# Performance work log

Hardware: AMD Instinct MI355X
Metric: run time of the kernel (lower is better)

## Reference

```python
import jax, jax.numpy as jnp
import numpy as np

OUT = 7  # STN crop size hard-coded as (7, 7) in the original build()


def gather_pairs(num_points):
    # replicates the pred_gather_indexes construction in build()
    pairs = [[0, 0]]
    si = 1
    while si + 2 < num_points:
        pairs.append([si, si])
        pairs.append([si + 1, si + 2])
        si += 3
    pairs.append([si, si])
    pairs.append([si + 1, si + 1])
    return np.asarray(pairs, dtype=np.int32)


def _sample_one(feat, theta):
    # feat [H,W,C], theta [6] = affine row-major 2x3; classic STN bilinear crop
    H, W, _ = feat.shape
    lin = jnp.linspace(-1.0, 1.0, OUT)
    gy, gx = jnp.meshgrid(lin, lin, indexing='ij')
    xs = theta[0] * gx + theta[1] * gy + theta[2]
    ys = theta[3] * gx + theta[4] * gy + theta[5]
    px = (xs + 1.0) * (W - 1) * 0.5
    py = (ys + 1.0) * (H - 1) * 0.5
    x0 = jnp.floor(px)
    y0 = jnp.floor(py)
    wx = px - x0
    wy = py - y0
    x0i = jnp.clip(x0, 0, W - 1).astype(jnp.int32)
    x1i = jnp.clip(x0 + 1, 0, W - 1).astype(jnp.int32)
    y0i = jnp.clip(y0, 0, H - 1).astype(jnp.int32)
    y1i = jnp.clip(y0 + 1, 0, H - 1).astype(jnp.int32)
    Ia = feat[y0i, x0i]
    Ib = feat[y1i, x0i]
    Ic = feat[y0i, x1i]
    Id = feat[y1i, x1i]
    wa = ((1 - wx) * (1 - wy))[..., None]
    wb = ((1 - wx) * wy)[..., None]
    wc = (wx * (1 - wy))[..., None]
    wd = (wx * wy)[..., None]
    return wa * Ia + wb * Ib + wc * Ic + wd * Id  # [OUT,OUT,C]

# vmap over boxes then over batch -> feat [B,H,W,C], theta [B,n,6] -> [B,n,7,7,C]
_sample = jax.vmap(jax.vmap(_sample_one, in_axes=(None, 0)), in_axes=(0, 0))


def _hierarchy(pred_prev, feat, W1, b1, W2, b2, W3, b3):
    B = pred_prev.shape[0]
    centers = (pred_prev[:, :-1] + pred_prev[:, 1:]) * 0.5
    diffs = (pred_prev[:, 1:] - pred_prev[:, :-1]) * 0.5
    cx, cy = centers[..., 0], centers[..., 1]
    dx, dy = diffs[..., 0], diffs[..., 1]
    # fixed (non-trainable) dense with constant kernel -> theta = [dx,-dy,-cx,dy,dx,-cy]
    theta = jnp.stack([dx, -dy, -cx, dy, dx, -cy], axis=-1)  # [B,n,6]
    theta = jax.lax.stop_gradient(theta)  # stop_gradient=True default
    rois = _sample(feat, theta)  # [B,n,7,7,C]
    n = theta.shape[1]
    x = rois.reshape(B * n, -1)
    f1 = jnp.tanh(x @ W1 + b1)
    f2 = jnp.tanh(f1 @ W2 + b2)
    f3 = f2 @ W3 + b3 + jnp.asarray([-1.0, 0.0, 0.0, 0.0, 1.0, 0.0], dtype=f2.dtype)
    npnt = n * 3
    pts = f3.reshape(B, npnt, 2)
    # fixed homography dense: (x,y) -> (x,y,-1)
    hom = jnp.concatenate([pts, -jnp.ones((B, npnt, 1), dtype=pts.dtype)], axis=-1)
    theta_e = jnp.repeat(theta, 3, axis=1).reshape(B, npnt, 2, 3)
    pt = jnp.einsum('bpij,bpj->bpi', theta_e, hom)  # [B,npnt,2]
    idx = gather_pairs(npnt)  # [m,2]
    pg = pt[:, idx]  # [B,m,2,2]
    return pg.mean(axis=2)  # [B,m,2]


def setup_inputs() -> dict:
    key = jax.random.key(0)
    ks = jax.random.split(key, 16)
    B = 32
    d = {
        'last_feature': jax.random.normal(ks[0], (B, 4096), jnp.float32),
        'conv4_3': jax.random.normal(ks[1], (B, 28, 28, 512), jnp.float32),
        'conv3_3': jax.random.normal(ks[2], (B, 56, 56, 256), jnp.float32),
        'conv2_2': jax.random.normal(ks[3], (B, 112, 112, 128), jnp.float32),
        'W_trans': jax.random.normal(ks[4], (4096, 18), jnp.float32) * 0.005,
        'b_trans': jnp.zeros((18,), jnp.float32),
    }
    C = [512, 256, 128]
    for h in range(3):
        kk = jax.random.split(ks[5 + h], 3)
        fan = OUT * OUT * C[h]
        d[f'W1_{h}'] = jax.random.normal(kk[0], (fan, 1024), jnp.float32) * 0.001
        d[f'b1_{h}'] = jnp.zeros((1024,), jnp.float32)
        d[f'W2_{h}'] = jax.random.normal(kk[1], (1024, 256), jnp.float32) * 0.02
        d[f'b2_{h}'] = jnp.zeros((256,), jnp.float32)
        d[f'W3_{h}'] = jax.random.normal(kk[2], (256, 6), jnp.float32) * 0.01
        d[f'b3_{h}'] = jnp.zeros((6,), jnp.float32)
    return d


def reference(last_feature, conv4_3, conv3_3, conv2_2, W_trans, b_trans,
              W1_0, b1_0, W2_0, b2_0, W3_0, b3_0,
              W1_1, b1_1, W2_1, b2_1, W3_1, b3_1,
              W1_2, b1_2, W2_2, b2_2, W3_2, b3_2):
    B = last_feature.shape[0]
    pred = (last_feature @ W_trans + b_trans).reshape(B, 9, 2)
    feats = [conv4_3, conv3_3, conv2_2]
    heads = [(W1_0, b1_0, W2_0, b2_0, W3_0, b3_0),
             (W1_1, b1_1, W2_1, b2_1, W3_1, b3_1),
             (W1_2, b1_2, W2_2, b2_2, W3_2, b3_2)]
    for h in range(3):
        pred = _hierarchy(pred, feats[h], *heads[h])
    return pred[:, :-1, :] * 6.0  # [B,64,2]
```

## Files before the change

kernel.cpp:

```cpp
#include <hip/hip_runtime.h>
#include <hip/hip_bf16.h>
#include <math.h>

typedef __attribute__((ext_vector_type(8))) short   short8;
typedef __attribute__((ext_vector_type(4))) float   floatx4;

#define OFF_PRED     0ULL
#define OFF_PTA      16384ULL
#define OFF_PTB      65536ULL
#define OFF_W2T      131072ULL
#define OFF_F1       2097152ULL
#define OFF_P2       4194304ULL
#define OFF_X        16777216ULL
#define OFF_P1       33554432ULL
#define OFF_W1T      67108864ULL

__device__ inline void pair_idx(int p, int Pn, int npnt, int& i1, int& i2) {
    if (p == 0) { i1 = i2 = 0; }
    else if (p >= Pn - 2) { i1 = i2 = npnt - (Pn - p); }
    else {
        int q = (p - 1) >> 1, r = (p - 1) & 1;
        int si = 1 + 3 * q;
        if (r == 0) { i1 = i2 = si; } else { i1 = si + 1; i2 = si + 2; }
    }
}
__device__ inline float2 pred_point(const float* pred0, const float* pt,
                                    int nsegP, int b, int p) {
    if (nsegP == 0) {
        const float* q = pred0 + ((size_t)b * 9 + p) * 2;
        return float2{q[0], q[1]};
    }
    int npnt = nsegP * 3, Pn = 2 * nsegP + 1;
    int i1, i2; pair_idx(p, Pn, npnt, i1, i2);
    const float* a = pt + ((size_t)b * npnt + i1) * 2;
    const float* c = pt + ((size_t)b * npnt + i2) * 2;
    return float2{0.5f * (a[0] + c[0]), 0.5f * (a[1] + c[1])};
}

struct SetupArgs {
    const float* W1s[3]; __hip_bfloat16* W1T[3]; int K[3];
    const float* W2s[3]; __hip_bfloat16* W2T[3];
    const float* lf; const float* Wt; const float* bt; float* pred;
};

__device__ inline void transpose_tile(const float* __restrict__ src,
                                      __hip_bfloat16* __restrict__ dst,
                                      int R, int C, int rowT, int colT,
                                      float (*tile)[33]) {
    int tx = threadIdx.x & 31, ty = threadIdx.x >> 5;
    int r0 = rowT * 32, c0 = colT * 32;
    #pragma unroll
    for (int k = 0; k < 4; ++k)
        tile[ty + k * 8][tx] = src[(size_t)(r0 + ty + k * 8) * C + c0 + tx];
    __syncthreads();
    #pragma unroll
    for (int k = 0; k < 4; ++k)
        dst[(size_t)(c0 + ty + k * 8) * R + r0 + tx] =
            __float2bfloat16(tile[tx][ty + k * 8]);
}

__global__ __launch_bounds__(256) void setup_kernel(SetupArgs a) {
    __shared__ float tile[32][33];
    int id = blockIdx.x;
    if (id < 43904) {
        int h = (id < 25088) ? 0 : (id < 37632 ? 1 : 2);
        int base = (h == 0) ? 0 : (h == 1 ? 25088 : 37632);
        int l = id - base;
        transpose_tile(a.W1s[h], a.W1T[h], a.K[h], 1024, l >> 5, l & 31, tile);
    } else if (id < 44672) {
        int l = id - 43904;
        int h = l >> 8; int t = l & 255;
        transpose_tile(a.W2s[h], a.W2T[h], 1024, 256, t >> 3, t & 7, tile);
    } else {
        int l = id - 44672;
        int wave = threadIdx.x >> 6, lane = threadIdx.x & 63;
        int task = l * 4 + wave;
        int j = task % 18, b = task / 18;
        const float* lfb = a.lf + (size_t)b * 4096;
        float acc = 0.f;
        for (int k = lane; k < 4096; k += 64)
            acc += lfb[k] * a.Wt[(size_t)k * 18 + j];
        #pragma unroll
        for (int off = 32; off >= 1; off >>= 1)
            acc += __shfl_xor(acc, off, 64);
        if (lane == 0) a.pred[b * 18 + j] = acc + a.bt[j];
    }
}

__global__ __launch_bounds__(256) void sample_kernel(
    const float* __restrict__ feat, int Wd, int lc,
    const float* __restrict__ pred0, const float* __restrict__ ptPrev, int nsegP,
    int lns, __hip_bfloat16* __restrict__ x)
{
    int nseg = 1 << lns;
    int blk = blockIdx.x;
    int i = blk & (nseg - 1), b = blk >> lns;
    float2 p0 = pred_point(pred0, ptPrev, nsegP, b, i);
    float2 p1 = pred_point(pred0, ptPrev, nsegP, b, i + 1);
    float cx = 0.5f * (p0.x + p1.x), cy = 0.5f * (p0.y + p1.y);
    float dx = 0.5f * (p1.x - p0.x), dy = 0.5f * (p1.y - p0.y);

    __shared__ float4 wv[49];
    __shared__ int4   ov[49];
    int t = threadIdx.x;
    int C = 1 << lc;
    if (t < 49) {
        int oy = t / 7, ox = t - oy * 7;
        float gx = (float)(ox - 3) * (1.f / 3.f);
        float gy = (float)(oy - 3) * (1.f / 3.f);
        float xs = dx * gx - dy * gy - cx;
        float ys = dy * gx + dx * gy - cy;
        float fW = (float)(Wd - 1);
        float px = (xs + 1.f) * fW * 0.5f;
        float py = (ys + 1.f) * fW * 0.5f;
        float x0f = floorf(px), y0f = floorf(py);
        float wx = px - x0f, wy = py - y0f;
        int xi0 = (int)fminf(fmaxf(x0f,       0.f), fW);
        int xi1 = (int)fminf(fmaxf(x0f + 1.f, 0.f), fW);
        int yi0 = (int)fminf(fmaxf(y0f,       0.f), fW);
        int yi1 = (int)fminf(fmaxf(y0f + 1.f, 0.f), fW);
        int c4 = C >> 2;
        ov[t] = int4{(yi0 * Wd + xi0) * c4, (yi1 * Wd + xi0) * c4,
                     (yi0 * Wd + xi1) * c4, (yi1 * Wd + xi1) * c4};
        wv[t] = float4{(1.f - wx) * (1.f - wy), (1.f - wx) * wy,
                       wx * (1.f - wy),         wx * wy};
    }
    __syncthreads();

    const float4* fb4 = (const float4*)(feat + (size_t)b * Wd * Wd * C);
    int c4 = 1 << (lc - 2);
    int total4 = 49 << (lc - 2);
    size_t rowbase = (size_t)blk * (49 << lc);
    for (int j = t; j < total4; j += 256) {
        int pix = j >> (lc - 2);
        int cc  = j & (c4 - 1);
        int4 o = ov[pix]; float4 w = wv[pix];
        float4 Ia = fb4[o.x + cc], Ib = fb4[o.y + cc];
        float4 Ic = fb4[o.z + cc], Id = fb4[o.w + cc];
        float4 v;
        v.x = w.x * Ia.x + w.y * Ib.x + w.z * Ic.x + w.w * Id.x;
        v.y = w.x * Ia.y + w.y * Ib.y + w.z * Ic.y + w.w * Id.y;
        v.z = w.x * Ia.z + w.y * Ib.z + w.z * Ic.z + w.w * Id.z;
        v.w = w.x * Ia.w + w.y * Ib.w + w.z * Ic.w + w.w * Id.w;
        __hip_bfloat16 h0 = __float2bfloat16(v.x), h1 = __float2bfloat16(v.y);
        __hip_bfloat16 h2 = __float2bfloat16(v.z), h3 = __float2bfloat16(v.w);
        ushort4 u = {*(unsigned short*)&h0, *(unsigned short*)&h1,
                     *(unsigned short*)&h2, *(unsigned short*)&h3};
        *(ushort4*)(x + rowbase + ((size_t)pix << lc) + cc * 4) = u;
    }
}

__global__ __launch_bounds__(256) void gemm_mfma4(
    const __hip_bfloat16* __restrict__ A, const __hip_bfloat16* __restrict__ Bt,
    float* __restrict__ P, int M, int N, int K, int slice)
{
    int lane = threadIdx.x & 63;
    int wave = threadIdx.x >> 6;
    int lo = lane & 15, hi = lane >> 4;
    int mt = blockIdx.x, nt = blockIdx.y * 4 + wave, s = blockIdx.z;
    const short* Ap = (const short*)A + (size_t)(mt * 64 + lo) * K + (size_t)s * slice + hi * 8;
    const short* Bp = (const short*)Bt + (size_t)(nt * 64 + lo) * K + (size_t)s * slice + hi * 8;

    floatx4 acc[4][4];
    #pragma unroll
    for (int a = 0; a < 4; ++a)
        #pragma unroll
        for (int b = 0; b < 4; ++b)
            acc[a][b] = floatx4{0.f, 0.f, 0.f, 0.f};

    short8 ca[4], cb[4], na[4], nb[4];
    int nch = slice >> 5;

#define LDF(da, db, koff)                                                     \
    {                                                                         \
        _Pragma("unroll")                                                     \
        for (int q = 0; q < 4; ++q)                                           \
            da[q] = *(const short8*)(Ap + (size_t)q * 16 * K + (koff));       \
        _Pragma("unroll")                                                     \
        for (int q = 0; q < 4; ++q)                                           \
            db[q] = *(const short8*)(Bp + (size_t)q * 16 * K + (koff));       \
    }
#define MM(da, db)                                                            \
    {                                                                         \
        _Pragma("unroll")                                                     \
        for (int mi = 0; mi < 4; ++mi)                                        \
            _Pragma("unroll")                                                 \
            for (int ni = 0; ni < 4; ++ni)                                    \
                acc[mi][ni] = __builtin_amdgcn_mfma_f32_16x16x32_bf16(        \
                    da[mi], db[ni], acc[mi][ni], 0, 0, 0);                    \
    }

    LDF(ca, cb, 0)
    for (int c = 0; c + 1 < nch; c += 2) {
        LDF(na, nb, (c + 1) * 32)
        MM(ca, cb)
        if (c + 2 < nch) LDF(ca, cb, (c + 2) * 32)
        MM(na, nb)
    }
    if (nch & 1) MM(ca, cb)

    #pragma unroll
    for (int mi = 0; mi < 4; ++mi) {
        int row0 = mt * 64 + mi * 16 + hi * 4;
        #pragma unroll
        for (int ni = 0; ni < 4; ++ni) {
            int col = nt * 64 + ni * 16 + lo;
            #pragma unroll
            for (int r = 0; r < 4; ++r)
                P[((size_t)s * M + row0 + r) * N + col] = acc[mi][ni][r];
        }
    }
#undef LDF
#undef MM
}

__global__ __launch_bounds__(256) void reduce_tanh_kernel(
    const float* __restrict__ P1, const float* __restrict__ b1,
    __hip_bfloat16* __restrict__ f1, int M, int S)
{
    int e = blockIdx.x * 256 + threadIdx.x;
    int n = e & 1023;
    float v = b1[n];
    size_t stride = (size_t)M * 1024;
    for (int s = 0; s < S; ++s) v += P1[(size_t)s * stride + e];
    f1[e] = __float2bfloat16(tanhf(v));
}

__global__ __launch_bounds__(64) void gemm3pts_kernel(
    const float* __restrict__ P2, const float* __restrict__ b2,
    const float* __restrict__ W3, const float* __restrict__ b3,
    const float* __restrict__ pred0, const float* __restrict__ ptPrev, int nsegP,
    float* __restrict__ pt, int lns, int M)
{
    int m = blockIdx.x;
    int lane = threadIdx.x;
    int nseg = 1 << lns;
    float acc[6] = {0.f, 0.f, 0.f, 0.f, 0.f, 0.f};
    #pragma unroll
    for (int q = 0; q < 4; ++q) {
        int k = lane + q * 64;
        float v = b2[k];
        #pragma unroll
        for (int s = 0; s < 8; ++s)
            v += P2[((size_t)s * M + m) * 256 + k];
        v = tanhf(v);
        const float* w = W3 + (size_t)k * 6;
        #pragma unroll
        for (int j = 0; j < 6; ++j) acc[j] += v * w[j];
    }
    #pragma unroll
    for (int j = 0; j < 6; ++j)
        #pragma unroll
        for (int off = 32; off >= 1; off >>= 1)
            acc[j] += __shfl_xor(acc[j], off, 64);
    if (lane == 0) {
        int i = m & (nseg - 1);
        int b = m >> lns;
        float2 p0 = pred_point(pred0, ptPrev, nsegP, b, i);
        float2 p1 = pred_point(pred0, ptPrev, nsegP, b, i + 1);
        float cx = 0.5f * (p0.x + p1.x), cy = 0.5f * (p0.y + p1.y);
        float dx = 0.5f * (p1.x - p0.x), dy = 0.5f * (p1.y - p0.y);
        float f[6];
        #pragma unroll
        for (int j = 0; j < 6; ++j) f[j] = acc[j] + b3[j];
        f[0] -= 1.f;
        f[4] += 1.f;
        int npnt = nseg * 3;
        size_t base = ((size_t)b * npnt + 3 * i) * 2;
        #pragma unroll
        for (int s = 0; s < 3; ++s) {
            float px = f[2 * s], py = f[2 * s + 1];
            pt[base + 2 * s]     = dx * px - dy * py + cx;
            pt[base + 2 * s + 1] = dy * px + dx * py + cy;
        }
    }
}

__global__ __launch_bounds__(256) void pairs_final_kernel(
    const float* __restrict__ pt, float* __restrict__ outp, int nsegP)
{
    int npnt = nsegP * 3;
    int Pn = 2 * nsegP + 1;
    int idx = blockIdx.x * 256 + threadIdx.x;
    int total = 32 * Pn * 2;
    if (idx >= total) return;
    int c = idx & 1;
    int t = idx >> 1;
    int p = t % Pn, b = t / Pn;
    int i1, i2; pair_idx(p, Pn, npnt, i1, i2);
    float v = 0.5f * (pt[((size_t)b * npnt + i1) * 2 + c] +
                      pt[((size_t)b * npnt + i2) * 2 + c]);
    if (p < Pn - 1) outp[((size_t)b * (Pn - 1) + p) * 2 + c] = 6.f * v;
}

extern "C" void kernel_launch(void* const* d_in, const int* in_sizes, int n_in,
                              void* d_out, int out_size, void* d_ws, size_t ws_size,
                              hipStream_t stream) {
    (void)in_sizes; (void)n_in; (void)out_size; (void)ws_size;
    const float* feats[3] = {(const float*)d_in[1], (const float*)d_in[2], (const float*)d_in[3]};

    char* ws = (char*)d_ws;
    float* predA = (float*)(ws + OFF_PRED);
    float* ptA   = (float*)(ws + OFF_PTA);
    float* ptB   = (float*)(ws + OFF_PTB);
    __hip_bfloat16* f1 = (__hip_bfloat16*)(ws + OFF_F1);
    float* P2          = (float*)(ws + OFF_P2);
    __hip_bfloat16* xb = (__hip_bfloat16*)(ws + OFF_X);
    float* P1          = (float*)(ws + OFF_P1);

    const int Ks[3]  = {25088, 12544, 6272};
    const int S1s[3] = {28, 14, 7};
    const int lcs[3] = {9, 8, 7};
    const int Hs[3]  = {28, 56, 112};
    const int lnss[3] = {3, 4, 5};

    SetupArgs sa;
    size_t w1off = 0;
    for (int h = 0; h < 3; ++h) {
        sa.W1s[h] = (const float*)d_in[6 + 6 * h];
        sa.W1T[h] = (__hip_bfloat16*)(ws + OFF_W1T + w1off);
        sa.K[h]   = Ks[h];
        w1off += (size_t)Ks[h] * 1024 * 2;
        sa.W2s[h] = (const float*)d_in[8 + 6 * h];
        sa.W2T[h] = (__hip_bfloat16*)(ws + OFF_W2T + (size_t)h * 524288);
    }
    sa.lf = (const float*)d_in[0];
    sa.Wt = (const float*)d_in[4];
    sa.bt = (const float*)d_in[5];
    sa.pred = predA;

    setup_kernel<<<dim3(44816), 256, 0, stream>>>(sa);

    float* pts[2] = {ptA, ptB};
    const float* ptPrev = nullptr;
    int nsegP = 0;
    for (int h = 0; h < 3; ++h) {
        int lns = lnss[h], nseg = 1 << lns, M = 32 * nseg;
        int K = Ks[h], S1 = S1s[h];
        const float* b1 = (const float*)d_in[7 + 6 * h];
        const float* b2 = (const float*)d_in[9 + 6 * h];
        const float* W3 = (const float*)d_in[10 + 6 * h];
        const float* b3 = (const float*)d_in[11 + 6 * h];

        sample_kernel<<<dim3(32 * nseg), 256, 0, stream>>>(
            feats[h], Hs[h], lcs[h], predA, ptPrev, nsegP, lns, xb);

        gemm_mfma4<<<dim3(M / 64, 4, S1), 256, 0, stream>>>(
            xb, sa.W1T[h], P1, M, 1024, K, K / S1);

        reduce_tanh_kernel<<<dim3(M * 1024 / 256), 256, 0, stream>>>(P1, b1, f1, M, S1);

        gemm_mfma4<<<dim3(M / 64, 1, 8), 256, 0, stream>>>(
            f1, sa.W2T[h], P2, M, 256, 1024, 128);

        float* ptCur = pts[h & 1];
        gemm3pts_kernel<<<dim3(M), 64, 0, stream>>>(
            P2, b2, W3, b3, predA, ptPrev, nsegP, ptCur, lns, M);

        ptPrev = ptCur; nsegP = nseg;
    }

    pairs_final_kernel<<<dim3((32 * 65 * 2 + 255) / 256), 256, 0, stream>>>(
        ptA, (float*)d_out, 32);
}
```

Baseline: 773.7 us.

## Fuse split-K reduce, second GEMM and final projection into one tail kernel

Replaces the reduce_tanh kernel, the second MFMA GEMM and the gemm3pts kernel with a single tail kernel. Each block handles four rows, reducing the split-K partials with tanh into shared memory, doing the 1024x256 product with scalar FMAs on bf16 weights, and applying the 6-wide projection. The setup transpose of W1 moves to 64x64 tiles with paired bf16 stores, and W2 is only converted rather than transposed. This removes two launches and the global round-trips for f1 and P2, but the second GEMM now runs on plain FMAs instead of MFMA and every block re-reads the whole W2.

```diff
diff --git a/kernel.cpp b/kernel.cpp
--- a/kernel.cpp
+++ b/kernel.cpp
@@ -8,9 +8,7 @@
 #define OFF_PRED     0ULL
 #define OFF_PTA      16384ULL
 #define OFF_PTB      65536ULL
-#define OFF_W2T      131072ULL
-#define OFF_F1       2097152ULL
-#define OFF_P2       4194304ULL
+#define OFF_W2B      131072ULL
 #define OFF_X        16777216ULL
 #define OFF_P1       33554432ULL
 #define OFF_W1T      67108864ULL
@@ -39,41 +37,52 @@
 
 struct SetupArgs {
     const float* W1s[3]; __hip_bfloat16* W1T[3]; int K[3];
-    const float* W2s[3]; __hip_bfloat16* W2T[3];
+    const float* W2s[3]; __hip_bfloat16* W2B[3];
     const float* lf; const float* Wt; const float* bt; float* pred;
 };
 
-__device__ inline void transpose_tile(const float* __restrict__ src,
-                                      __hip_bfloat16* __restrict__ dst,
-                                      int R, int C, int rowT, int colT,
-                                      float (*tile)[33]) {
-    int tx = threadIdx.x & 31, ty = threadIdx.x >> 5;
-    int r0 = rowT * 32, c0 = colT * 32;
-    #pragma unroll
-    for (int k = 0; k < 4; ++k)
-        tile[ty + k * 8][tx] = src[(size_t)(r0 + ty + k * 8) * C + c0 + tx];
-    __syncthreads();
-    #pragma unroll
-    for (int k = 0; k < 4; ++k)
-        dst[(size_t)(c0 + ty + k * 8) * R + r0 + tx] =
-            __float2bfloat16(tile[tx][ty + k * 8]);
-}
-
 __global__ __launch_bounds__(256) void setup_kernel(SetupArgs a) {
-    __shared__ float tile[32][33];
+    __shared__ float tile[64][65];
     int id = blockIdx.x;
-    if (id < 43904) {
-        int h = (id < 25088) ? 0 : (id < 37632 ? 1 : 2);
-        int base = (h == 0) ? 0 : (h == 1 ? 25088 : 37632);
+    int t = threadIdx.x;
+    if (id < 10976) {
+        int h, base;
+        if (id < 6272) { h = 0; base = 0; }
+        else if (id < 9408) { h = 1; base = 6272; }
+        else { h = 2; base = 9408; }
         int l = id - base;
-        transpose_tile(a.W1s[h], a.W1T[h], a.K[h], 1024, l >> 5, l & 31, tile);
-    } else if (id < 44672) {
-        int l = id - 43904;
-        int h = l >> 8; int t = l & 255;
-        transpose_tile(a.W2s[h], a.W2T[h], 1024, 256, t >> 3, t & 7, tile);
+        int K = a.K[h];
+        const float* src = a.W1s[h];
+        __hip_bfloat16* dst = a.W1T[h];
+        int r0 = (l >> 4) * 64, c0 = (l & 15) * 64;
+        int col = t & 63, row4 = t >> 6;
+        #pragma unroll
+        for (int g = 0; g < 16; ++g)
+            tile[row4 + g * 4][col] =
+                src[(size_t)(r0 + row4 + g * 4) * 1024 + c0 + col];
+        __syncthreads();
+        int ox = t & 31, oy = t >> 5;
+        #pragma unroll
+        for (int g = 0; g < 8; ++g) {
+            int n = oy + g * 8;
+            __hip_bfloat16 h0 = __float2bfloat16(tile[ox * 2][n]);
+            __hip_bfloat16 h1 = __float2bfloat16(tile[ox * 2 + 1][n]);
+            ushort2 u = {*(unsigned short*)&h0, *(unsigned short*)&h1};
+            *(ushort2*)((unsigned short*)dst + (size_t)(c0 + n) * K + r0 + ox * 2) = u;
+        }
+    } else if (id < 11744) {
+        int l = id - 10976;
+        int h = l >> 8, blk = l & 255;
+        int idx = blk * 1024 + t * 4;
+        float4 v = *(const float4*)(a.W2s[h] + idx);
+        __hip_bfloat16 h0 = __float2bfloat16(v.x), h1 = __float2bfloat16(v.y);
+        __hip_bfloat16 h2 = __float2bfloat16(v.z), h3 = __float2bfloat16(v.w);
+        ushort4 u = {*(unsigned short*)&h0, *(unsigned short*)&h1,
+                     *(unsigned short*)&h2, *(unsigned short*)&h3};
+        *(ushort4*)((unsigned short*)a.W2B[h] + idx) = u;
     } else {
-        int l = id - 44672;
-        int wave = threadIdx.x >> 6, lane = threadIdx.x & 63;
+        int l = id - 11744;
+        int wave = t >> 6, lane = t & 63;
         int task = l * 4 + wave;
         int j = task % 18, b = task / 18;
         const float* lfb = a.lf + (size_t)b * 4096;
@@ -214,55 +223,101 @@
 #undef MM
 }
 
-__global__ __launch_bounds__(256) void reduce_tanh_kernel(
+__global__ __launch_bounds__(256) void tail_kernel(
     const float* __restrict__ P1, const float* __restrict__ b1,
-    __hip_bfloat16* __restrict__ f1, int M, int S)
-{
-    int e = blockIdx.x * 256 + threadIdx.x;
-    int n = e & 1023;
-    float v = b1[n];
-    size_t stride = (size_t)M * 1024;
-    for (int s = 0; s < S; ++s) v += P1[(size_t)s * stride + e];
-    f1[e] = __float2bfloat16(tanhf(v));
-}
-
-__global__ __launch_bounds__(64) void gemm3pts_kernel(
-    const float* __restrict__ P2, const float* __restrict__ b2,
+    const __hip_bfloat16* __restrict__ W2B, const float* __restrict__ b2,
     const float* __restrict__ W3, const float* __restrict__ b3,
     const float* __restrict__ pred0, const float* __restrict__ ptPrev, int nsegP,
-    float* __restrict__ pt, int lns, int M)
+    float* __restrict__ pt, int lns, int M, int S)
 {
-    int m = blockIdx.x;
-    int lane = threadIdx.x;
-    int nseg = 1 << lns;
-    float acc[6] = {0.f, 0.f, 0.f, 0.f, 0.f, 0.f};
+    __shared__ float f1s[4 * 1024];
+    __shared__ float red[4][24];
+    __shared__ float fin[24];
+    int t = threadIdx.x;
+    int m0 = blockIdx.x * 4;
+
+    float4 bv = ((const float4*)b1)[t];
     #pragma unroll
     for (int q = 0; q < 4; ++q) {
-        int k = lane + q * 64;
-        float v = b2[k];
-        #pragma unroll
-        for (int s = 0; s < 8; ++s)
-            v += P2[((size_t)s * M + m) * 256 + k];
-        v = tanhf(v);
-        const float* w = W3 + (size_t)k * 6;
-        #pragma unroll
-        for (int j = 0; j < 6; ++j) acc[j] += v * w[j];
-    }
-    #pragma unroll
-    for (int j = 0; j < 6; ++j)
-        #pragma unroll
-        for (int off = 32; off >= 1; off >>= 1)
-            acc[j] += __shfl_xor(acc[j], off, 64);
+        float4 v = bv;
+        for (int s = 0; s < S; ++s) {
+            float4 p = ((const float4*)(P1 + ((size_t)s * M + m0 + q) * 1024))[t];
+            v.x += p.x; v.y += p.y; v.z += p.z; v.w += p.w;
+        }
+        float4 o = {tanhf(v.x), tanhf(v.y), tanhf(v.z), tanhf(v.w)};
+        ((float4*)(f1s + q * 1024))[t] = o;
+    }
+    __syncthreads();
+
+    int kq = t & 63, jq = t >> 6;
+    float acc[4][4];
+    #pragma unroll
+    for (int q = 0; q < 4; ++q)
+        #pragma unroll
+        for (int r = 0; r < 4; ++r) acc[q][r] = 0.f;
+    for (int j = jq * 256; j < jq * 256 + 256; ++j) {
+        ushort4 w = *(const ushort4*)((const unsigned short*)W2B + (size_t)j * 256 + kq * 4);
+        float w0 = __uint_as_float((unsigned)w.x << 16);
+        float w1 = __uint_as_float((unsigned)w.y << 16);
+        float w2 = __uint_as_float((unsigned)w.z << 16);
+        float w3 = __uint_as_float((unsigned)w.w << 16);
+        #pragma unroll
+        for (int q = 0; q < 4; ++q) {
+            float f = f1s[q * 1024 + j];
+            acc[q][0] += f * w0; acc[q][1] += f * w1;
+            acc[q][2] += f * w2; acc[q][3] += f * w3;
+        }
+    }
+    __syncthreads();
+    #pragma unroll
+    for (int q = 0; q < 4; ++q)
+        ((float4*)f1s)[(jq * 64 + kq) * 4 + q] =
+            float4{acc[q][0], acc[q][1], acc[q][2], acc[q][3]};
+    __syncthreads();
+
+    int kq2 = t >> 2, ks = t & 3;
+    float vv[4];
+    float bb = b2[t];
+    #pragma unroll
+    for (int q = 0; q < 4; ++q) {
+        float s4 = 0.f;
+        #pragma unroll
+        for (int j2 = 0; j2 < 4; ++j2)
+            s4 += f1s[((j2 * 64 + kq2) * 4 + q) * 4 + ks];
+        vv[q] = tanhf(s4 + bb);
+    }
+
+    float w6[6];
+    #pragma unroll
+    for (int j = 0; j < 6; ++j) w6[j] = W3[t * 6 + j];
+    float a[24];
+    #pragma unroll
+    for (int q = 0; q < 4; ++q)
+        #pragma unroll
+        for (int j = 0; j < 6; ++j) a[q * 6 + j] = vv[q] * w6[j];
+    #pragma unroll
+    for (int off = 32; off >= 1; off >>= 1)
+        #pragma unroll
+        for (int e = 0; e < 24; ++e) a[e] += __shfl_xor(a[e], off, 64);
+    int wave = t >> 6, lane = t & 63;
     if (lane == 0) {
-        int i = m & (nseg - 1);
-        int b = m >> lns;
+        #pragma unroll
+        for (int e = 0; e < 24; ++e) red[wave][e] = a[e];
+    }
+    __syncthreads();
+    if (t < 24) fin[t] = red[0][t] + red[1][t] + red[2][t] + red[3][t];
+    __syncthreads();
+    if (t < 4) {
+        int m = m0 + t;
+        int nseg = 1 << lns;
+        int i = m & (nseg - 1), b = m >> lns;
         float2 p0 = pred_point(pred0, ptPrev, nsegP, b, i);
         float2 p1 = pred_point(pred0, ptPrev, nsegP, b, i + 1);
         float cx = 0.5f * (p0.x + p1.x), cy = 0.5f * (p0.y + p1.y);
         float dx = 0.5f * (p1.x - p0.x), dy = 0.5f * (p1.y - p0.y);
         float f[6];
         #pragma unroll
-        for (int j = 0; j < 6; ++j) f[j] = acc[j] + b3[j];
+        for (int j = 0; j < 6; ++j) f[j] = fin[t * 6 + j] + b3[j];
         f[0] -= 1.f;
         f[4] += 1.f;
         int npnt = nseg * 3;
@@ -303,15 +358,13 @@
     float* predA = (float*)(ws + OFF_PRED);
     float* ptA   = (float*)(ws + OFF_PTA);
     float* ptB   = (float*)(ws + OFF_PTB);
-    __hip_bfloat16* f1 = (__hip_bfloat16*)(ws + OFF_F1);
-    float* P2          = (float*)(ws + OFF_P2);
     __hip_bfloat16* xb = (__hip_bfloat16*)(ws + OFF_X);
     float* P1          = (float*)(ws + OFF_P1);
 
-    const int Ks[3]  = {25088, 12544, 6272};
-    const int S1s[3] = {28, 14, 7};
-    const int lcs[3] = {9, 8, 7};
-    const int Hs[3]  = {28, 56, 112};
+    const int Ks[3]   = {25088, 12544, 6272};
+    const int S1s[3]  = {28, 14, 7};
+    const int lcs[3]  = {9, 8, 7};
+    const int Hs[3]   = {28, 56, 112};
     const int lnss[3] = {3, 4, 5};
 
     SetupArgs sa;
@@ -322,14 +375,14 @@
         sa.K[h]   = Ks[h];
         w1off += (size_t)Ks[h] * 1024 * 2;
         sa.W2s[h] = (const float*)d_in[8 + 6 * h];
-        sa.W2T[h] = (__hip_bfloat16*)(ws + OFF_W2T + (size_t)h * 524288);
+        sa.W2B[h] = (__hip_bfloat16*)(ws + OFF_W2B + (size_t)h * 524288);
     }
     sa.lf = (const float*)d_in[0];
     sa.Wt = (const float*)d_in[4];
     sa.bt = (const float*)d_in[5];
     sa.pred = predA;
 
-    setup_kernel<<<dim3(44816), 256, 0, stream>>>(sa);
+    setup_kernel<<<dim3(11888), 256, 0, stream>>>(sa);
 
     float* pts[2] = {ptA, ptB};
     const float* ptPrev = nullptr;
@@ -348,14 +401,10 @@
         gemm_mfma4<<<dim3(M / 64, 4, S1), 256, 0, stream>>>(
             xb, sa.W1T[h], P1, M, 1024, K, K / S1);
 
-        reduce_tanh_kernel<<<dim3(M * 1024 / 256), 256, 0, stream>>>(P1, b1, f1, M, S1);
-
-        gemm_mfma4<<<dim3(M / 64, 1, 8), 256, 0, stream>>>(
-            f1, sa.W2T[h], P2, M, 256, 1024, 128);
-
         float* ptCur = pts[h & 1];
-        gemm3pts_kernel<<<dim3(M), 64, 0, stream>>>(
-            P2, b2, W3, b3, predA, ptPrev, nsegP, ptCur, lns, M);
+        tail_kernel<<<dim3(M / 4), 256, 0, stream>>>(
+            P1, b1, sa.W2B[h], b2, W3, b3, predA, ptPrev, nsegP,
+            ptCur, lns, M, S1);
 
         ptPrev = ptCur; nsegP = nseg;
     }
```

Result: slower. 846.9 us (+9.5%).
